# Kernel optimization log

Measured on AMD Instinct MI355X. Metric: run time of the kernel, lower is better.

## Reference

```python
import jax, jax.numpy as jnp
import numpy as np

N = 100000   # nodes
E = 1600000  # directed edges
NF = 128     # n_feat
NH = 128     # n_hid
NC = 64      # n_class


def _glorot(key, fan_in, fan_out):
    lim = (6.0 / (fan_in + fan_out)) ** 0.5
    return jax.random.uniform(key, (fan_in, fan_out), dtype=jnp.float32, minval=-lim, maxval=lim)


def setup_inputs() -> dict:
    key = jax.random.key(0)
    ks = jax.random.split(key, 10)
    x = jax.random.normal(ks[0], (N, NF), dtype=jnp.float32)
    edge_index = jax.random.randint(ks[1], (2, E), 0, N, dtype=jnp.int32)
    return {
        "x": x,
        "edge_index": edge_index,
        "W_in": _glorot(ks[2], NF, NH),
        "b_in": jnp.zeros((NH,), jnp.float32),
        "W_mid0": _glorot(ks[3], NH, NH),
        "b_mid0": jnp.zeros((NH,), jnp.float32),
        "W_mid1": _glorot(ks[4], NH, NH),
        "b_mid1": jnp.zeros((NH,), jnp.float32),
        "W_out": _glorot(ks[5], NH, NC),
        "b_out": jnp.zeros((NC,), jnp.float32),
        "W_skip_out": _glorot(ks[6], NH, NC),
    }


def _gcn_conv(x, W, b, src, dst, coef, n):
    # x' = D^-1/2 (A + I) D^-1/2 (x W) + b   (symmetric-normalized GCN conv)
    h = x @ W                               # [N, out]
    msg = h[src] * coef[:, None]            # [E+N, out] gather + scale
    return jax.ops.segment_sum(msg, dst, num_segments=n) + b


def reference(x, edge_index, W_in, b_in, W_mid0, b_mid0, W_mid1, b_mid1, W_out, b_out, W_skip_out):
    loops = jnp.arange(N, dtype=edge_index.dtype)
    src = jnp.concatenate([edge_index[0], loops])  # add self-loops
    dst = jnp.concatenate([edge_index[1], loops])
    deg = jax.ops.segment_sum(jnp.ones_like(dst, dtype=jnp.float32), dst, num_segments=N)
    dinv = jax.lax.rsqrt(deg)                      # deg >= 1 due to self-loops
    coef = dinv[src] * dinv[dst]                   # [E+N]

    # in layer: conv + res skip (NF == NH so plain add) + relu; dropout is no-op in eval
    h = _gcn_conv(x, W_in, b_in, src, dst, coef, N)
    x = jax.nn.relu(h + x)
    # mid layers
    for W, b in ((W_mid0, b_mid0), (W_mid1, b_mid1)):
        h = _gcn_conv(x, W, b, src, dst, coef, N)
        x = jax.nn.relu(h + x)
    # out layer: conv + res skip with channel projection NH -> NC
    h = _gcn_conv(x, W_out, b_out, src, dst, coef, N)
    return h + x @ W_skip_out
```

## Files before the change

### kernel.cpp

```cpp
#include <hip/hip_runtime.h>
#include <hip/hip_bf16.h>

constexpr int NN = 100000;
constexpr int NE = 1600000;
constexpr int BKN  = 256;
constexpr int NB2  = (NN + BKN - 1) / BKN;
constexpr int TILE = 4096;
constexpr int NT   = (NE + TILE - 1) / TILE;

__device__ __forceinline__ unsigned short f2bf(float f) {
    unsigned int u = __float_as_uint(f);
    unsigned int r = (u + 0x7fffu + ((u >> 16) & 1u)) >> 16;
    return (unsigned short)r;
}
__device__ __forceinline__ float bflo(unsigned int u) { return __uint_as_float(u << 16); }
__device__ __forceinline__ float bfhi(unsigned int u) { return __uint_as_float(u & 0xffff0000u); }
__device__ __forceinline__ float bf2f(unsigned short h) { return __uint_as_float(((unsigned int)h) << 16); }
__device__ __forceinline__ unsigned int pack2bf(float lo, float hi) {
    return (unsigned int)f2bf(lo) | ((unsigned int)f2bf(hi) << 16);
}

typedef __bf16 v8bf __attribute__((ext_vector_type(8)));
typedef float  v4f  __attribute__((ext_vector_type(4)));
typedef float  v2f  __attribute__((ext_vector_type(2)));

__device__ __forceinline__ v2f fp8x2_to_f32(unsigned int u) {
    v2f t = __builtin_amdgcn_cvt_pk_f32_fp8(u, false);
    return t;
}
__device__ __forceinline__ float fp8b(unsigned char b) {
    v2f t = __builtin_amdgcn_cvt_pk_f32_fp8((unsigned int)b, false);
    return t.x;
}

constexpr size_t OFF_BCNT  = 0;
constexpr size_t OFF_BBASE = OFF_BCNT  + 2048;
constexpr size_t OFF_BCUR  = OFF_BBASE + 2048;
constexpr size_t OFF_RP    = OFF_BCUR  + 2048;
constexpr size_t OFF_DINV  = OFF_RP    + 400384;
constexpr size_t OFF_COL   = OFF_DINV  + 400384;
constexpr size_t OFF_WT    = OFF_COL   + 6400000;
constexpr size_t OFF_H8    = OFF_WT    + 32768;
constexpr size_t OFF_H     = OFF_H8    + 12800000;
constexpr size_t OFF_X     = OFF_H     + 25600000;


__global__ __launch_bounds__(256) void bhist_kernel(const int* __restrict__ edst,
                                                    int* __restrict__ bcnt) {
    __shared__ int h[NB2];
    for (int i = threadIdx.x; i < NB2; i += 256) h[i] = 0;
    __syncthreads();
    const int base = blockIdx.x * TILE;
    #pragma unroll
    for (int j = 0; j < 16; ++j) {
        int e = base + j * 256 + threadIdx.x;
        if (e < NE) atomicAdd(&h[edst[e] >> 8], 1);
    }
    __syncthreads();
    for (int i = threadIdx.x; i < NB2; i += 256)
        if (h[i]) atomicAdd(&bcnt[i], h[i]);
}

__global__ __launch_bounds__(512) void bscan_kernel(const int* __restrict__ bcnt,
                                                    int* __restrict__ bbase,
                                                    int* __restrict__ bcur) {
    __shared__ int s[512];
    const int t = threadIdx.x;
    int v = (t < NB2) ? bcnt[t] : 0;
    s[t] = v;
    __syncthreads();
    for (int off = 1; off < 512; off <<= 1) {
        int a = (t >= off) ? s[t - off] : 0;
        __syncthreads();
        s[t] += a;
        __syncthreads();
    }
    int excl = s[t] - v;
    if (t < NB2) { bbase[t] = excl; bcur[t] = excl; }
    if (t == NB2 - 1) bbase[NB2] = excl + v;
}

__global__ __launch_bounds__(256) void scatter2_kernel(const int* __restrict__ esrc,
                                                       const int* __restrict__ edst,
                                                       int* __restrict__ bcur,
                                                       unsigned int* __restrict__ ebuf) {
    __shared__ int h[NB2];
    __shared__ int cur[NB2];
    for (int i = threadIdx.x; i < NB2; i += 256) h[i] = 0;
    __syncthreads();
    const int base = blockIdx.x * TILE;
    #pragma unroll
    for (int j = 0; j < 16; ++j) {
        int e = base + j * 256 + threadIdx.x;
        if (e < NE) atomicAdd(&h[edst[e] >> 8], 1);
    }
    __syncthreads();
    for (int i = threadIdx.x; i < NB2; i += 256) {
        int c = h[i];
        cur[i] = c ? atomicAdd(&bcur[i], c) : 0;
    }
    __syncthreads();
    #pragma unroll
    for (int j = 0; j < 16; ++j) {
        int e = base + j * 256 + threadIdx.x;
        if (e < NE) {
            int s = esrc[e], d = edst[e];
            int pos = atomicAdd(&cur[d >> 8], 1);
            ebuf[pos] = (unsigned int)s | ((unsigned int)(d & 255) << 24);
        }
    }
}

__global__ __launch_bounds__(256) void csrfill2_kernel(const unsigned int* __restrict__ ebuf,
                                                       const int* __restrict__ bbase,
                                                       int* __restrict__ rp,
                                                       float* __restrict__ dinv,
                                                       int* __restrict__ col) {
    __shared__ int cnt[256];
    __shared__ int cursor[256];
    __shared__ int s[256];
    __shared__ int sbeg, send;
    const int b = blockIdx.x;
    const int t = threadIdx.x;
    if (t == 0) { sbeg = bbase[b]; send = bbase[b + 1]; }
    cnt[t] = 0;
    __syncthreads();
    const int beg = sbeg, end = send;
    const int node0 = b * BKN;

    for (int e = beg + t; e < end; e += 256)
        atomicAdd(&cnt[ebuf[e] >> 24], 1);
    __syncthreads();

    int v = cnt[t];
    s[t] = v;
    __syncthreads();
    for (int off = 1; off < 256; off <<= 1) {
        int a = (t >= off) ? s[t - off] : 0;
        __syncthreads();
        s[t] += a;
        __syncthreads();
    }
    int excl = s[t] - v;
    int gnode = node0 + t;
    if (gnode < NN) {
        rp[gnode]   = beg + excl;
        dinv[gnode] = rsqrtf((float)(v + 1));
    }
    cursor[t] = beg + excl;
    if (b == NB2 - 1 && t == 0) rp[NN] = NE;
    __syncthreads();

    for (int e = beg + t; e < end; e += 256) {
        unsigned int sd = ebuf[e];
        int pos = atomicAdd(&cursor[sd >> 24], 1);
        col[pos] = (int)(sd & 0xFFFFFFu);
    }
}

__global__ __launch_bounds__(256) void wpre_kernel(const float* __restrict__ W0,
                                                   const float* __restrict__ W1,
                                                   int wstride,
                                                   unsigned short* __restrict__ Wt) {
    int e = blockIdx.x * 256 + threadIdx.x;
    int k = e >> 7, c = e & 127;
    float v = (c < 64) ? W0[(size_t)k * wstride + c] : W1[(size_t)k * wstride + (c - 64)];
    Wt[c * 128 + k] = f2bf(v);
}

constexpr int XROW = 136;

template<bool XF32, int OMODE>
__global__ __launch_bounds__(256) void gemm_mfma_kernel(const void* __restrict__ Xv,
                                                        const unsigned short* __restrict__ Wt,
                                                        const float* __restrict__ dinv,
                                                        int scaleMask,
                                                        void* __restrict__ Ho) {
    __shared__ unsigned short Wl[128 * XROW];
    __shared__ unsigned short Xl[64 * XROW];

    const int t = threadIdx.x;
    const int rowBase = blockIdx.x * 64;

    #pragma unroll
    for (int i = 0; i < 8; ++i) {
        int f = i * 256 + t;
        int r = f >> 4, c8 = f & 15;
        uint4 w = *(const uint4*)&Wt[r * 128 + c8 * 8];
        *(uint4*)&Wl[r * XROW + c8 * 8] = w;
    }
    if (XF32) {
        const float* X = (const float*)Xv;
        #pragma unroll
        for (int i = 0; i < 8; ++i) {
            int f = i * 256 + t;
            int r = f >> 5, c4 = f & 31;
            int gn = rowBase + r;
            float4 v = make_float4(0.f, 0.f, 0.f, 0.f);
            if (gn < NN) v = *(const float4*)&X[(size_t)gn * 128 + c4 * 4];
            ushort4 o;
            o.x = f2bf(v.x); o.y = f2bf(v.y); o.z = f2bf(v.z); o.w = f2bf(v.w);
            *(ushort4*)&Xl[r * XROW + c4 * 4] = o;
        }
    } else {
        const unsigned short* X = (const unsigned short*)Xv;
        #pragma unroll
        for (int i = 0; i < 4; ++i) {
            int f = i * 256 + t;
            int r = f >> 4, c8 = f & 15;
            int gn = rowBase + r;
            uint4 v = make_uint4(0u, 0u, 0u, 0u);
            if (gn < NN) v = *(const uint4*)&X[(size_t)gn * 128 + c8 * 8];
            *(uint4*)&Xl[r * XROW + c8 * 8] = v;
        }
    }
    __syncthreads();

    const int w  = t >> 6;
    const int l  = t & 63;
    const int lr = l & 15;
    const int lk = (l >> 4) * 8;

    v4f acc[8];
    #pragma unroll
    for (int n = 0; n < 8; ++n) acc[n] = (v4f){0.f, 0.f, 0.f, 0.f};

    const unsigned short* ax = &Xl[(w * 16 + lr) * XROW + lk];
    const unsigned short* bx = &Wl[lr * XROW + lk];

    #pragma unroll
    for (int kk = 0; kk < 4; ++kk) {
        v8bf a = *(const v8bf*)&ax[kk * 32];
        #pragma unroll
        for (int n = 0; n < 8; ++n) {
            v8bf b = *(const v8bf*)&bx[(n * 16) * XROW + kk * 32];
            acc[n] = __builtin_amdgcn_mfma_f32_16x16x32_bf16(a, b, acc[n], 0, 0, 0);
        }
    }

    #pragma unroll
    for (int r_ = 0; r_ < 4; ++r_) {
        int row  = w * 16 + (l >> 4) * 4 + r_;
        int grow = rowBase + row;
        float dsc = dinv[grow < NN ? grow : NN - 1];
        #pragma unroll
        for (int n = 0; n < 8; ++n) {
            float sc = ((scaleMask >> (n >> 2)) & 1) ? dsc : 1.f;
            Xl[row * XROW + n * 16 + lr] = f2bf(acc[n][r_] * sc);
        }
    }
    __syncthreads();

    if (OMODE == 1) {
        unsigned char* H8 = (unsigned char*)Ho;
        #pragma unroll
        for (int i = 0; i < 4; ++i) {
            int f = i * 256 + t;
            int r = f >> 4, c8 = f & 15;
            int gn = rowBase + r;
            if (gn < NN) {
                uint4 v = *(const uint4*)&Xl[r * XROW + c8 * 8];
                unsigned int lo = __builtin_amdgcn_cvt_pk_fp8_f32(bflo(v.x), bfhi(v.x), 0u, false);
                lo = __builtin_amdgcn_cvt_pk_fp8_f32(bflo(v.y), bfhi(v.y), lo, true);
                unsigned int hi = __builtin_amdgcn_cvt_pk_fp8_f32(bflo(v.z), bfhi(v.z), 0u, false);
                hi = __builtin_amdgcn_cvt_pk_fp8_f32(bflo(v.w), bfhi(v.w), hi, true);
                *(uint2*)&H8[(size_t)gn * 128 + c8 * 8] = make_uint2(lo, hi);
            }
        }
    } else {
        unsigned char*  h8o   = (unsigned char*)Ho;
        unsigned short* skipb = (unsigned short*)((char*)Ho + (size_t)NN * 64);
        #pragma unroll
        for (int i = 0; i < 4; ++i) {
            int f = i * 256 + t;
            int r = f >> 4, c8 = f & 15;
            int gn = rowBase + r;
            if (gn < NN) {
                uint4 v = *(const uint4*)&Xl[r * XROW + c8 * 8];
                if (c8 < 8) {
                    unsigned int lo = __builtin_amdgcn_cvt_pk_fp8_f32(bflo(v.x), bfhi(v.x), 0u, false);
                    lo = __builtin_amdgcn_cvt_pk_fp8_f32(bflo(v.y), bfhi(v.y), lo, true);
                    unsigned int hi = __builtin_amdgcn_cvt_pk_fp8_f32(bflo(v.z), bfhi(v.z), 0u, false);
                    hi = __builtin_amdgcn_cvt_pk_fp8_f32(bflo(v.w), bfhi(v.w), hi, true);
                    *(uint2*)&h8o[(size_t)gn * 64 + c8 * 8] = make_uint2(lo, hi);
                } else {
                    *(uint4*)&skipb[(size_t)gn * 64 + (c8 - 8) * 8] = v;
                }
            }
        }
    }
}

template<bool XF32>
__global__ __launch_bounds__(256) void agg128_kernel(const unsigned char* __restrict__ H8,
                                                     const void* __restrict__ Xoldv,
                                                     const int* __restrict__ rp,
                                                     const int* __restrict__ col,
                                                     const float* __restrict__ dinv,
                                                     const float* __restrict__ bias,
                                                     unsigned int* __restrict__ Xnew) {
    const int wid  = threadIdx.x >> 6;
    const int lane = threadIdx.x & 63;
    const int i = blockIdx.x * 4 + wid;
    if (i >= NN) return;

    const unsigned short* __restrict__ Hs = (const unsigned short*)H8;

    const float di = dinv[i];
    const float2 b2 = ((const float2*)bias)[lane];
    float xox, xoy;
    if (XF32) {
        float2 xo = ((const float2*)Xoldv)[(size_t)i * 64 + lane];
        xox = xo.x; xoy = xo.y;
    } else {
        unsigned int xo = ((const unsigned int*)Xoldv)[(size_t)i * 64 + lane];
        xox = bflo(xo); xoy = bfhi(xo);
    }

    v2f sf = fp8x2_to_f32(Hs[(size_t)i * 64 + lane]);
    float ax = sf.x, ay = sf.y;

    const int beg = rp[i], end = rp[i + 1];
    int e = beg;
    for (; e + 16 <= end; e += 16) {
        unsigned int u[16];
        #pragma unroll
        for (int j = 0; j < 16; ++j) u[j] = Hs[(size_t)col[e + j] * 64 + lane];
        v2f m[16];
        #pragma unroll
        for (int j = 0; j < 16; ++j) m[j] = fp8x2_to_f32(u[j]);
        v2f s01 = ((m[0] + m[1]) + (m[2] + m[3])) + ((m[4] + m[5]) + (m[6] + m[7]));
        v2f s02 = ((m[8] + m[9]) + (m[10] + m[11])) + ((m[12] + m[13]) + (m[14] + m[15]));
        ax += s01.x + s02.x;
        ay += s01.y + s02.y;
    }
    for (; e + 4 <= end; e += 4) {
        unsigned int u0 = Hs[(size_t)col[e]     * 64 + lane];
        unsigned int u1 = Hs[(size_t)col[e + 1] * 64 + lane];
        unsigned int u2 = Hs[(size_t)col[e + 2] * 64 + lane];
        unsigned int u3 = Hs[(size_t)col[e + 3] * 64 + lane];
        v2f m0 = fp8x2_to_f32(u0), m1 = fp8x2_to_f32(u1);
        v2f m2 = fp8x2_to_f32(u2), m3 = fp8x2_to_f32(u3);
        ax += (m0.x + m1.x) + (m2.x + m3.x);
        ay += (m0.y + m1.y) + (m2.y + m3.y);
    }
    for (; e < end; ++e) {
        v2f m = fp8x2_to_f32(Hs[(size_t)col[e] * 64 + lane]);
        ax += m.x;
        ay += m.y;
    }

    float ox = fmaxf(di * ax + b2.x + xox, 0.f);
    float oy = fmaxf(di * ay + b2.y + xoy, 0.f);
    Xnew[(size_t)i * 64 + lane] = pack2bf(ox, oy);
}

__global__ __launch_bounds__(256) void aggout_kernel(const unsigned char* __restrict__ h8o,
                                                     const unsigned short* __restrict__ skipb,
                                                     const int* __restrict__ rp,
                                                     const int* __restrict__ col,
                                                     const float* __restrict__ dinv,
                                                     const float* __restrict__ bias,
                                                     float* __restrict__ out) {
    const int wid  = threadIdx.x >> 6;
    const int lane = threadIdx.x & 63;
    const int i = blockIdx.x * 4 + wid;
    if (i >= NN) return;

    const float di = dinv[i];
    const float b  = bias[lane];
    const float sk = bf2f(skipb[(size_t)i * 64 + lane]);

    float a = fp8b(h8o[(size_t)i * 64 + lane]);
    const int beg = rp[i], end = rp[i + 1];
    int e = beg;
    for (; e + 8 <= end; e += 8) {
        unsigned char c0 = h8o[(size_t)col[e]     * 64 + lane];
        unsigned char c1 = h8o[(size_t)col[e + 1] * 64 + lane];
        unsigned char c2 = h8o[(size_t)col[e + 2] * 64 + lane];
        unsigned char c3 = h8o[(size_t)col[e + 3] * 64 + lane];
        unsigned char c4 = h8o[(size_t)col[e + 4] * 64 + lane];
        unsigned char c5 = h8o[(size_t)col[e + 5] * 64 + lane];
        unsigned char c6 = h8o[(size_t)col[e + 6] * 64 + lane];
        unsigned char c7 = h8o[(size_t)col[e + 7] * 64 + lane];
        a += ((fp8b(c0) + fp8b(c1)) + (fp8b(c2) + fp8b(c3))) +
             ((fp8b(c4) + fp8b(c5)) + (fp8b(c6) + fp8b(c7)));
    }
    for (; e + 4 <= end; e += 4) {
        unsigned char c0 = h8o[(size_t)col[e]     * 64 + lane];
        unsigned char c1 = h8o[(size_t)col[e + 1] * 64 + lane];
        unsigned char c2 = h8o[(size_t)col[e + 2] * 64 + lane];
        unsigned char c3 = h8o[(size_t)col[e + 3] * 64 + lane];
        a += (fp8b(c0) + fp8b(c1)) + (fp8b(c2) + fp8b(c3));
    }
    for (; e < end; ++e) a += fp8b(h8o[(size_t)col[e] * 64 + lane]);

    out[(size_t)i * 64 + lane] = di * a + b + sk;
}

extern "C" void kernel_launch(void* const* d_in, const int* in_sizes, int n_in,
                              void* d_out, int out_size, void* d_ws, size_t ws_size,
                              hipStream_t stream) {
    const float* x      = (const float*)d_in[0];
    const int*   ei     = (const int*)d_in[1];
    const float* W_in   = (const float*)d_in[2];
    const float* b_in   = (const float*)d_in[3];
    const float* W_mid0 = (const float*)d_in[4];
    const float* b_mid0 = (const float*)d_in[5];
    const float* W_mid1 = (const float*)d_in[6];
    const float* b_mid1 = (const float*)d_in[7];
    const float* W_out  = (const float*)d_in[8];
    const float* b_out  = (const float*)d_in[9];
    const float* W_skip = (const float*)d_in[10];

    const int* esrc = ei;
    const int* edst = ei + NE;

    char* ws = (char*)d_ws;
    int*   bcnt   = (int*)  (ws + OFF_BCNT);
    int*   bbase  = (int*)  (ws + OFF_BBASE);
    int*   bcur   = (int*)  (ws + OFF_BCUR);
    int*   rp     = (int*)  (ws + OFF_RP);
    float* dinv   = (float*)(ws + OFF_DINV);
    int*   col    = (int*)  (ws + OFF_COL);
    unsigned short* wt   = (unsigned short*)(ws + OFF_WT);
    unsigned char*  h8   = (unsigned char*) (ws + OFF_H8);
    unsigned char*  h8o  = (unsigned char*) (ws + OFF_H);
    unsigned short* skipb = (unsigned short*)(ws + OFF_H + (size_t)NN * 64);
    unsigned int*   ebuf = (unsigned int*)  (ws + OFF_H);
    unsigned short* xbuf = (unsigned short*)(ws + OFF_X);
    unsigned int*   xbufw = (unsigned int*) (ws + OFF_X);
    float* outp   = (float*)d_out;

    const int gemmGrid = (NN + 63) / 64;
    const int aggGrid  = (NN + 3) / 4;

    (void)hipMemsetAsync(bcnt, 0, (size_t)(NB2 + 1) * 4, stream);
    bhist_kernel<<<NT, 256, 0, stream>>>(edst, bcnt);
    bscan_kernel<<<1, 512, 0, stream>>>(bcnt, bbase, bcur);
    scatter2_kernel<<<NT, 256, 0, stream>>>(esrc, edst, bcur, ebuf);
    csrfill2_kernel<<<NB2, 256, 0, stream>>>(ebuf, bbase, rp, dinv, col);

    wpre_kernel<<<64, 256, 0, stream>>>(W_in, W_in + 64, 128, wt);
    gemm_mfma_kernel<true, 1><<<gemmGrid, 256, 0, stream>>>(x, wt, dinv, 3, h8);
    agg128_kernel<true><<<aggGrid, 256, 0, stream>>>(h8, x, rp, col, dinv, b_in, xbufw);

    wpre_kernel<<<64, 256, 0, stream>>>(W_mid0, W_mid0 + 64, 128, wt);
    gemm_mfma_kernel<false, 1><<<gemmGrid, 256, 0, stream>>>(xbuf, wt, dinv, 3, h8);
    agg128_kernel<false><<<aggGrid, 256, 0, stream>>>(h8, xbuf, rp, col, dinv, b_mid0, xbufw);

    wpre_kernel<<<64, 256, 0, stream>>>(W_mid1, W_mid1 + 64, 128, wt);
    gemm_mfma_kernel<false, 1><<<gemmGrid, 256, 0, stream>>>(xbuf, wt, dinv, 3, h8);
    agg128_kernel<false><<<aggGrid, 256, 0, stream>>>(h8, xbuf, rp, col, dinv, b_mid1, xbufw);

    wpre_kernel<<<64, 256, 0, stream>>>(W_out, W_skip, 64, wt);
    gemm_mfma_kernel<false, 2><<<gemmGrid, 256, 0, stream>>>(xbuf, wt, dinv, 1, (void*)h8o);
    aggout_kernel<<<aggGrid, 256, 0, stream>>>(h8o, skipb, rp, col, dinv, b_out, outp);
}
```

Before: 340.2 us.

## Stage bucketed edges in shared memory and shrink aggregation unroll to eight

The bucket scatter kernel now keeps edge values in registers, computes per-bucket local offsets with a block prefix scan, sorts edges into a shared-memory staging buffer, and then writes them to global memory in contiguous runs per bucket. This replaces scattered per-edge global writes and drops the second read of the edge arrays. Separately, the mid-layer aggregation gather loop is unrolled by 8 instead of 16, which lowers register pressure but leaves fewer loads in flight per thread. The staging adds about 24KB of shared memory per block, which may reduce occupancy of the scatter kernel.

```diff
diff --git a/kernel.cpp b/kernel.cpp
--- a/kernel.cpp
+++ b/kernel.cpp
@@ -85,29 +85,69 @@
                                                        int* __restrict__ bcur,
                                                        unsigned int* __restrict__ ebuf) {
     __shared__ int h[NB2];
-    __shared__ int cur[NB2];
-    for (int i = threadIdx.x; i < NB2; i += 256) h[i] = 0;
-    __syncthreads();
+    __shared__ int loff[NB2];
+    __shared__ int gbase[NB2];
+    __shared__ int sc[512];
+    __shared__ unsigned int   stage[TILE];
+    __shared__ unsigned short sbkt[TILE];
+    const int t = threadIdx.x;
     const int base = blockIdx.x * TILE;
+
+    for (int i = t; i < NB2; i += 256) h[i] = 0;
+    __syncthreads();
+
+    int es[16], ed[16];
     #pragma unroll
     for (int j = 0; j < 16; ++j) {
-        int e = base + j * 256 + threadIdx.x;
-        if (e < NE) atomicAdd(&h[edst[e] >> 8], 1);
-    }
-    __syncthreads();
-    for (int i = threadIdx.x; i < NB2; i += 256) {
-        int c = h[i];
-        cur[i] = c ? atomicAdd(&bcur[i], c) : 0;
-    }
-    __syncthreads();
+        int e = base + j * 256 + t;
+        if (e < NE) {
+            es[j] = esrc[e];
+            ed[j] = edst[e];
+            atomicAdd(&h[ed[j] >> 8], 1);
+        } else {
+            es[j] = -1; ed[j] = 0;
+        }
+    }
+    __syncthreads();
+
+    sc[t]       = (t < NB2)       ? h[t]       : 0;
+    sc[t + 256] = (t + 256 < NB2) ? h[t + 256] : 0;
+    __syncthreads();
+    for (int off = 1; off < 512; off <<= 1) {
+        int a0 = (t >= off)       ? sc[t - off]       : 0;
+        int a1 = (t + 256 >= off) ? sc[t + 256 - off] : 0;
+        __syncthreads();
+        sc[t] += a0; sc[t + 256] += a1;
+        __syncthreads();
+    }
+    if (t < NB2) {
+        loff[t]  = sc[t] - h[t];
+        gbase[t] = h[t] ? atomicAdd(&bcur[t], h[t]) : 0;
+    }
+    if (t + 256 < NB2) {
+        loff[t + 256]  = sc[t + 256] - h[t + 256];
+        gbase[t + 256] = h[t + 256] ? atomicAdd(&bcur[t + 256], h[t + 256]) : 0;
+    }
+    __syncthreads();
+    for (int i = t; i < NB2; i += 256) h[i] = 0;
+    __syncthreads();
+
     #pragma unroll
     for (int j = 0; j < 16; ++j) {
-        int e = base + j * 256 + threadIdx.x;
-        if (e < NE) {
-            int s = esrc[e], d = edst[e];
-            int pos = atomicAdd(&cur[d >> 8], 1);
-            ebuf[pos] = (unsigned int)s | ((unsigned int)(d & 255) << 24);
-        }
+        if (es[j] >= 0) {
+            int b = ed[j] >> 8;
+            int r = atomicAdd(&h[b], 1);
+            int slot = loff[b] + r;
+            stage[slot] = (unsigned int)es[j] | ((unsigned int)(ed[j] & 255) << 24);
+            sbkt[slot]  = (unsigned short)b;
+        }
+    }
+    __syncthreads();
+
+    int nval = NE - base; if (nval > TILE) nval = TILE;
+    for (int j = t; j < nval; j += 256) {
+        int b = sbkt[j];
+        ebuf[gbase[b] + (j - loff[b])] = stage[j];
     }
 }
 
@@ -322,23 +362,30 @@
 
     const int beg = rp[i], end = rp[i + 1];
     int e = beg;
-    for (; e + 16 <= end; e += 16) {
-        unsigned int u[16];
-        #pragma unroll
-        for (int j = 0; j < 16; ++j) u[j] = Hs[(size_t)col[e + j] * 64 + lane];
-        v2f m[16];
-        #pragma unroll
-        for (int j = 0; j < 16; ++j) m[j] = fp8x2_to_f32(u[j]);
-        v2f s01 = ((m[0] + m[1]) + (m[2] + m[3])) + ((m[4] + m[5]) + (m[6] + m[7]));
-        v2f s02 = ((m[8] + m[9]) + (m[10] + m[11])) + ((m[12] + m[13]) + (m[14] + m[15]));
-        ax += s01.x + s02.x;
-        ay += s01.y + s02.y;
+    for (; e + 8 <= end; e += 8) {
+        int s0 = col[e],     s1 = col[e + 1], s2 = col[e + 2], s3 = col[e + 3];
+        int s4 = col[e + 4], s5 = col[e + 5], s6 = col[e + 6], s7 = col[e + 7];
+        unsigned int u0 = Hs[(size_t)s0 * 64 + lane];
+        unsigned int u1 = Hs[(size_t)s1 * 64 + lane];
+        unsigned int u2 = Hs[(size_t)s2 * 64 + lane];
+        unsigned int u3 = Hs[(size_t)s3 * 64 + lane];
+        unsigned int u4 = Hs[(size_t)s4 * 64 + lane];
+        unsigned int u5 = Hs[(size_t)s5 * 64 + lane];
+        unsigned int u6 = Hs[(size_t)s6 * 64 + lane];
+        unsigned int u7 = Hs[(size_t)s7 * 64 + lane];
+        v2f m0 = fp8x2_to_f32(u0), m1 = fp8x2_to_f32(u1);
+        v2f m2 = fp8x2_to_f32(u2), m3 = fp8x2_to_f32(u3);
+        v2f m4 = fp8x2_to_f32(u4), m5 = fp8x2_to_f32(u5);
+        v2f m6 = fp8x2_to_f32(u6), m7 = fp8x2_to_f32(u7);
+        ax += ((m0.x + m1.x) + (m2.x + m3.x)) + ((m4.x + m5.x) + (m6.x + m7.x));
+        ay += ((m0.y + m1.y) + (m2.y + m3.y)) + ((m4.y + m5.y) + (m6.y + m7.y));
     }
     for (; e + 4 <= end; e += 4) {
-        unsigned int u0 = Hs[(size_t)col[e]     * 64 + lane];
-        unsigned int u1 = Hs[(size_t)col[e + 1] * 64 + lane];
-        unsigned int u2 = Hs[(size_t)col[e + 2] * 64 + lane];
-        unsigned int u3 = Hs[(size_t)col[e + 3] * 64 + lane];
+        int s0 = col[e], s1 = col[e + 1], s2 = col[e + 2], s3 = col[e + 3];
+        unsigned int u0 = Hs[(size_t)s0 * 64 + lane];
+        unsigned int u1 = Hs[(size_t)s1 * 64 + lane];
+        unsigned int u2 = Hs[(size_t)s2 * 64 + lane];
+        unsigned int u3 = Hs[(size_t)s3 * 64 + lane];
         v2f m0 = fp8x2_to_f32(u0), m1 = fp8x2_to_f32(u1);
         v2f m2 = fp8x2_to_f32(u2), m3 = fp8x2_to_f32(u3);
         ax += (m0.x + m1.x) + (m2.x + m3.x);
```

Result: no change. 335.8 us (-1.3%).
